# Kernel tuning notes

Measured on AMD Instinct MI355X. Metric: run time of the kernel, lower is better.

Reference implementation:

```python
import jax, jax.numpy as jnp
import numpy as np

B, S, H, NH, L, NS = 8, 4096, 768, 12, 2, 64
DH = H // NH
EPS = 1e-12


def _layer_norm(x, g, b):
    mu = jnp.mean(x, axis=-1, keepdims=True)
    var = jnp.mean((x - mu) ** 2, axis=-1, keepdims=True)
    return (x - mu) / jnp.sqrt(var + EPS) * g + b


def setup_inputs() -> dict:
    key = jax.random.key(0)
    ks = jax.random.split(key, 8)
    # sentence index per token: 64 equal contiguous sentences; position 0 is [CLS] in sentence 0
    sent_ind = jnp.broadcast_to((jnp.arange(S, dtype=jnp.int32) * NS) // S, (B, S)).astype(jnp.int32)
    start_layer = jax.random.normal(ks[0], (B, S, H), dtype=jnp.float32)
    init = lambda k, shape: (jax.random.normal(k, shape, dtype=jnp.float32) * 0.02)
    return {
        "sent_ind": sent_ind,
        "start_layer": start_layer,
        "Wq": init(ks[1], (L, H, H)), "bq": jnp.zeros((L, H), jnp.float32),
        "Wk": init(ks[2], (L, H, H)), "bk": jnp.zeros((L, H), jnp.float32),
        "Wv": init(ks[3], (L, H, H)), "bv": jnp.zeros((L, H), jnp.float32),
        "Wo": init(ks[4], (L, H, H)), "bo": jnp.zeros((L, H), jnp.float32),
        "ln_g": jnp.ones((L, H), jnp.float32), "ln_b": jnp.zeros((L, H), jnp.float32),
    }


def reference(sent_ind, start_layer, Wq, bq, Wk, bk, Wv, bv, Wo, bo, ln_g, ln_b):
    # ---- segment-mean pooling by sentence index (vectorized replacement of the python loops) ----
    onehot = (sent_ind[..., None] == jnp.arange(NS, dtype=sent_ind.dtype)).astype(start_layer.dtype)  # [B,S,NS]
    # the first [CLS] token is excluded from sentence 0's mean
    onehot = onehot.at[:, 0, :].set(0.0)
    sums = jnp.einsum('bsn,bsd->bnd', onehot, start_layer)          # [B,NS,H]
    counts = jnp.sum(onehot, axis=1)                                 # [B,NS]
    x = sums / counts[..., None]                                     # graph_vectors [B,NS,H]

    # ---- GAT layers: BertSelfAttention + GATSelfOutput(dense->gelu->LayerNorm), dropout=eval ----
    scale = 1.0 / (DH ** 0.5)
    for i in range(L):
        q = (x @ Wq[i] + bq[i]).reshape(B, NS, NH, DH)
        k = (x @ Wk[i] + bk[i]).reshape(B, NS, NH, DH)
        v = (x @ Wv[i] + bv[i]).reshape(B, NS, NH, DH)
        scores = jnp.einsum('bqhd,bkhd->bhqk', q, k) * scale
        probs = jax.nn.softmax(scores, axis=-1)
        ctx = jnp.einsum('bhqk,bkhd->bqhd', probs, v).reshape(B, NS, H)
        h = jax.nn.gelu(ctx @ Wo[i] + bo[i], approximate=False)
        x = _layer_norm(h, ln_g[i], ln_b[i])
    return x
```

## Files before the change

### kernel.cpp

```cpp
#include <hip/hip_runtime.h>
#include <hip/hip_bf16.h>

constexpr int cB  = 8;
constexpr int cS  = 4096;
constexpr int cH  = 768;
constexpr int cNH = 12;
constexpr int cL  = 2;
constexpr int cNS = 64;
constexpr int cDH = 64;
constexpr int cM  = cB * cNS;

typedef __attribute__((ext_vector_type(8))) short bf16x8;
typedef __attribute__((ext_vector_type(4))) float f32x4;

union PrepShared {
    struct { int cnt; int list[cS]; float ps[192][4]; } p;
    float T[2][64][65];
};

__global__ __launch_bounds__(512) void prep_kernel(
    const int* __restrict__ sent_ind, const float* __restrict__ sl,
    __hip_bfloat16* __restrict__ xb,
    const float* __restrict__ Wq, const float* __restrict__ Wk,
    const float* __restrict__ Wv, const float* __restrict__ Wo,
    __hip_bfloat16* __restrict__ wt)
{
    __shared__ PrepShared sh;
    int tid = threadIdx.x;

    if (blockIdx.x < (unsigned)cM) {
        int bn = blockIdx.x;
        int b = bn >> 6, n = bn & (cNS - 1);
        if (tid == 0) sh.p.cnt = 0;
        __syncthreads();
        const int* si = sent_ind + (size_t)b * cS;
        for (int s = tid; s < cS; s += 512)
            if (s != 0 && si[s] == n) { int p = atomicAdd(&sh.p.cnt, 1); sh.p.list[p] = s; }
        __syncthreads();
        int c = sh.p.cnt;
        int grp = tid >> 8;
        int t   = tid & 255;
        int c0 = c >> 1;
        int lo = grp ? c0 : 0;
        int hi = grp ? c  : c0;
        float s0 = 0.f, s1 = 0.f, s2 = 0.f, s3 = 0.f;
        if (t < 192) {
            const float* bbase = sl + (size_t)b * cS * cH;
            int col = t * 4;
            float4 a0 = {0.f, 0.f, 0.f, 0.f};
            float4 a1 = {0.f, 0.f, 0.f, 0.f};
            float4 a2 = {0.f, 0.f, 0.f, 0.f};
            float4 a3 = {0.f, 0.f, 0.f, 0.f};
            int i = lo;
            for (; i + 4 <= hi; i += 4) {
                float4 r0 = *(const float4*)(bbase + (size_t)sh.p.list[i + 0] * cH + col);
                float4 r1 = *(const float4*)(bbase + (size_t)sh.p.list[i + 1] * cH + col);
                float4 r2 = *(const float4*)(bbase + (size_t)sh.p.list[i + 2] * cH + col);
                float4 r3 = *(const float4*)(bbase + (size_t)sh.p.list[i + 3] * cH + col);
                a0.x += r0.x; a0.y += r0.y; a0.z += r0.z; a0.w += r0.w;
                a1.x += r1.x; a1.y += r1.y; a1.z += r1.z; a1.w += r1.w;
                a2.x += r2.x; a2.y += r2.y; a2.z += r2.z; a2.w += r2.w;
                a3.x += r3.x; a3.y += r3.y; a3.z += r3.z; a3.w += r3.w;
            }
            for (; i < hi; ++i) {
                float4 r0 = *(const float4*)(bbase + (size_t)sh.p.list[i] * cH + col);
                a0.x += r0.x; a0.y += r0.y; a0.z += r0.z; a0.w += r0.w;
            }
            s0 = a0.x + a1.x + a2.x + a3.x;
            s1 = a0.y + a1.y + a2.y + a3.y;
            s2 = a0.z + a1.z + a2.z + a3.z;
            s3 = a0.w + a1.w + a2.w + a3.w;
        }
        if (grp == 1 && t < 192) {
            sh.p.ps[t][0] = s0; sh.p.ps[t][1] = s1;
            sh.p.ps[t][2] = s2; sh.p.ps[t][3] = s3;
        }
        __syncthreads();
        if (grp == 0 && t < 192) {
            float inv = 1.0f / (float)c;
            __hip_bfloat16* xr = xb + (size_t)bn * cH + t * 4;
            xr[0] = __float2bfloat16((s0 + sh.p.ps[t][0]) * inv);
            xr[1] = __float2bfloat16((s1 + sh.p.ps[t][1]) * inv);
            xr[2] = __float2bfloat16((s2 + sh.p.ps[t][2]) * inv);
            xr[3] = __float2bfloat16((s3 + sh.p.ps[t][3]) * inv);
        }
    } else {
        int sub = tid >> 8;
        int t   = tid & 255;
        int bi = (blockIdx.x - cM) * 2 + sub;
        int bx = bi % 12, by = (bi / 12) % 12, mat = bi / 144;
        int layer = mat >> 2, which = mat & 3;
        const float* W = (which == 0 ? Wq : which == 1 ? Wk : which == 2 ? Wv : Wo)
                         + (size_t)layer * cH * cH;
        int k0 = by * 64, n0 = bx * 64;
        int r = t >> 2, cb = (t & 3) * 16;
        #pragma unroll
        for (int u = 0; u < 4; ++u) {
            float4 w4 = *(const float4*)(W + (size_t)(k0 + r) * cH + n0 + cb + u * 4);
            sh.T[sub][r][cb + u * 4 + 0] = w4.x; sh.T[sub][r][cb + u * 4 + 1] = w4.y;
            sh.T[sub][r][cb + u * 4 + 2] = w4.z; sh.T[sub][r][cb + u * 4 + 3] = w4.w;
        }
        __syncthreads();
        int nn = t >> 2, kseg = (t & 3) * 16;
        __hip_bfloat16 tmp[16] __attribute__((aligned(16)));
        #pragma unroll
        for (int j = 0; j < 16; ++j)
            tmp[j] = __float2bfloat16(sh.T[sub][kseg + j][nn]);
        __hip_bfloat16* dst = wt + ((size_t)mat * cH + n0 + nn) * cH + k0 + kseg;
        *(bf16x8*)(dst)     = *(const bf16x8*)(tmp);
        *(bf16x8*)(dst + 8) = *(const bf16x8*)(tmp + 8);
    }
}

struct AttnShared {
    float QP[cNS][cDH + 4];
    float Ks[cNS][cDH + 4];
    float Vt[cDH][cNS + 4];
};

__global__ __launch_bounds__(256) void qkvattn_kernel(
    const __hip_bfloat16* __restrict__ x_bf,
    const __hip_bfloat16* __restrict__ wqkv,
    const float* __restrict__ bq, const float* __restrict__ bk,
    const float* __restrict__ bv,
    __hip_bfloat16* __restrict__ ctx_bf)
{
    __shared__ AttnShared sh;
    int tid = threadIdx.x;
    int lane = tid & 63, wave = tid >> 6;
    int l15 = lane & 15, q4 = lane >> 4;
    int b = blockIdx.x / cNH, hh = blockIdx.x % cNH;

    const __hip_bfloat16* Arow[4];
    #pragma unroll
    for (int m = 0; m < 4; ++m)
        Arow[m] = x_bf + (size_t)(b * 64 + m * 16 + l15) * cH + q4 * 8;
    const __hip_bfloat16* Brow[3];
    int cmat[3], cnt_[3];
    #pragma unroll
    for (int j = 0; j < 3; ++j) {
        int c = wave * 3 + j;
        cmat[j] = c >> 2; cnt_[j] = c & 3;
        Brow[j] = wqkv + (size_t)cmat[j] * cH * cH
                       + (size_t)(hh * 64 + cnt_[j] * 16 + l15) * cH + q4 * 8;
    }

    f32x4 acc[3][4];
    #pragma unroll
    for (int j = 0; j < 3; ++j)
        #pragma unroll
        for (int m = 0; m < 4; ++m) acc[j][m] = (f32x4){0.f, 0.f, 0.f, 0.f};

    #pragma unroll 4
    for (int k0 = 0; k0 < cH; k0 += 32) {
        bf16x8 a[4], bb8[3];
        #pragma unroll
        for (int m = 0; m < 4; ++m) a[m] = *(const bf16x8*)(Arow[m] + k0);
        #pragma unroll
        for (int j = 0; j < 3; ++j) bb8[j] = *(const bf16x8*)(Brow[j] + k0);
        #pragma unroll
        for (int j = 0; j < 3; ++j)
            #pragma unroll
            for (int m = 0; m < 4; ++m)
                acc[j][m] = __builtin_amdgcn_mfma_f32_16x16x32_bf16(a[m], bb8[j], acc[j][m], 0, 0, 0);
    }

    const float scale = 0.125f;
    #pragma unroll
    for (int j = 0; j < 3; ++j) {
        int mat = cmat[j], nt = cnt_[j];
        int col_d = nt * 16 + l15;
        int col_g = hh * 64 + col_d;
        float bias = (mat == 0 ? bq : mat == 1 ? bk : bv)[col_g];
        #pragma unroll
        for (int m = 0; m < 4; ++m) {
            #pragma unroll
            for (int r = 0; r < 4; ++r) {
                int row_s = m * 16 + q4 * 4 + r;
                float v = acc[j][m][r] + bias;
                if (mat == 0)      sh.QP[row_s][col_d] = v * scale;
                else if (mat == 1) sh.Ks[row_s][col_d] = v;
                else               sh.Vt[col_d][row_s] = v;
            }
        }
    }
    __syncthreads();

    int tx = tid & 15, ty = tid >> 4;
    float accs[4][4] = {};
    for (int d = 0; d < cDH; d += 4) {
        float4 qv[4], kv[4];
        #pragma unroll
        for (int i = 0; i < 4; ++i) qv[i] = *(const float4*)&sh.QP[ty * 4 + i][d];
        #pragma unroll
        for (int j = 0; j < 4; ++j) kv[j] = *(const float4*)&sh.Ks[tx + j * 16][d];
        #pragma unroll
        for (int i = 0; i < 4; ++i)
            #pragma unroll
            for (int j = 0; j < 4; ++j)
                accs[i][j] += qv[i].x * kv[j].x + qv[i].y * kv[j].y +
                              qv[i].z * kv[j].z + qv[i].w * kv[j].w;
    }
    __syncthreads();
    #pragma unroll
    for (int i = 0; i < 4; ++i)
        #pragma unroll
        for (int j = 0; j < 4; ++j)
            sh.QP[ty * 4 + i][tx + j * 16] = accs[i][j];
    __syncthreads();

    {
        int row = tid >> 2, jq = tid & 3;
        float e[16];
        float m = -1e30f;
        #pragma unroll
        for (int c = 0; c < 16; ++c) { e[c] = sh.QP[row][jq * 16 + c]; m = fmaxf(m, e[c]); }
        m = fmaxf(m, __shfl_xor(m, 1));
        m = fmaxf(m, __shfl_xor(m, 2));
        float s = 0.f;
        #pragma unroll
        for (int c = 0; c < 16; ++c) { e[c] = __expf(e[c] - m); s += e[c]; }
        s += __shfl_xor(s, 1);
        s += __shfl_xor(s, 2);
        float inv = 1.0f / s;
        #pragma unroll
        for (int c = 0; c < 16; ++c) sh.QP[row][jq * 16 + c] = e[c] * inv;
    }
    __syncthreads();

    float acco[4][4] = {};
    for (int c = 0; c < cNS; c += 4) {
        float4 p4[4], vt4[4];
        #pragma unroll
        for (int i = 0; i < 4; ++i) p4[i] = *(const float4*)&sh.QP[ty * 4 + i][c];
        #pragma unroll
        for (int j = 0; j < 4; ++j) vt4[j] = *(const float4*)&sh.Vt[tx + j * 16][c];
        #pragma unroll
        for (int i = 0; i < 4; ++i)
            #pragma unroll
            for (int j = 0; j < 4; ++j)
                acco[i][j] += p4[i].x * vt4[j].x + p4[i].y * vt4[j].y +
                              p4[i].z * vt4[j].z + p4[i].w * vt4[j].w;
    }
    size_t base = ((size_t)b * cNS) * cH + hh * cDH;
    #pragma unroll
    for (int i = 0; i < 4; ++i)
        #pragma unroll
        for (int j = 0; j < 4; ++j)
            ctx_bf[base + (size_t)(ty * 4 + i) * cH + tx + j * 16] =
                __float2bfloat16(acco[i][j]);
}

__global__ __launch_bounds__(256) void ogemm_kernel(
    const __hip_bfloat16* __restrict__ A,
    const __hip_bfloat16* __restrict__ Wt,
    const float* __restrict__ bias,
    __hip_bfloat16* __restrict__ C)
{
    int lane = threadIdx.x & 63;
    int wave = threadIdx.x >> 6;
    int l15 = lane & 15, q4 = lane >> 4;
    int m0 = blockIdx.y * 64 + wave * 16;
    int n0 = blockIdx.x * 32;

    const __hip_bfloat16* Arow = A  + (size_t)(m0 + l15) * cH + q4 * 8;
    const __hip_bfloat16* Wr0  = Wt + (size_t)(n0 + l15) * cH + q4 * 8;
    const __hip_bfloat16* Wr1  = Wr0 + (size_t)16 * cH;

    f32x4 acc0 = {0.f, 0.f, 0.f, 0.f};
    f32x4 acc1 = {0.f, 0.f, 0.f, 0.f};
    #pragma unroll 8
    for (int k0 = 0; k0 < cH; k0 += 32) {
        bf16x8 a  = *(const bf16x8*)(Arow + k0);
        bf16x8 b0 = *(const bf16x8*)(Wr0 + k0);
        bf16x8 b1 = *(const bf16x8*)(Wr1 + k0);
        acc0 = __builtin_amdgcn_mfma_f32_16x16x32_bf16(a, b0, acc0, 0, 0, 0);
        acc1 = __builtin_amdgcn_mfma_f32_16x16x32_bf16(a, b1, acc1, 0, 0, 0);
    }
    #pragma unroll
    for (int nt = 0; nt < 2; ++nt) {
        const f32x4 acc = nt == 0 ? acc0 : acc1;
        int col = n0 + nt * 16 + l15;
        float bv = bias[col];
        #pragma unroll
        for (int r = 0; r < 4; ++r) {
            float v = acc[r] + bv;
            v = 0.5f * v * (1.0f + erff(v * 0.70710678118654752f));
            C[(size_t)(m0 + q4 * 4 + r) * cH + col] = __float2bfloat16(v);
        }
    }
}

__global__ __launch_bounds__(256) void ln_kernel(
    const __hip_bfloat16* __restrict__ h, const float* __restrict__ g,
    const float* __restrict__ bb, __hip_bfloat16* __restrict__ xb,
    float* __restrict__ outf)
{
    int row = blockIdx.x;
    const __hip_bfloat16* r = h + (size_t)row * cH;
    int tid = threadIdx.x;
    float v0 = __bfloat162float(r[tid]);
    float v1 = __bfloat162float(r[tid + 256]);
    float v2 = __bfloat162float(r[tid + 512]);
    float s = v0 + v1 + v2;
    __shared__ float red[4];
    #pragma unroll
    for (int o = 32; o; o >>= 1) s += __shfl_xor(s, o);
    if ((tid & 63) == 0) red[tid >> 6] = s;
    __syncthreads();
    float mu = (red[0] + red[1] + red[2] + red[3]) * (1.0f / 768.0f);
    float d0 = v0 - mu, d1 = v1 - mu, d2 = v2 - mu;
    float ss = d0 * d0 + d1 * d1 + d2 * d2;
    __syncthreads();
    #pragma unroll
    for (int o = 32; o; o >>= 1) ss += __shfl_xor(ss, o);
    if ((tid & 63) == 0) red[tid >> 6] = ss;
    __syncthreads();
    float var = (red[0] + red[1] + red[2] + red[3]) * (1.0f / 768.0f);
    float inv = rsqrtf(var + 1e-12f);
    float o0 = d0 * inv * g[tid]       + bb[tid];
    float o1 = d1 * inv * g[tid + 256] + bb[tid + 256];
    float o2 = d2 * inv * g[tid + 512] + bb[tid + 512];
    __hip_bfloat16* xr = xb + (size_t)row * cH;
    xr[tid]       = __float2bfloat16(o0);
    xr[tid + 256] = __float2bfloat16(o1);
    xr[tid + 512] = __float2bfloat16(o2);
    if (outf) {
        float* orow = outf + (size_t)row * cH;
        orow[tid] = o0; orow[tid + 256] = o1; orow[tid + 512] = o2;
    }
}

extern "C" void kernel_launch(void* const* d_in, const int* in_sizes, int n_in,
                              void* d_out, int out_size, void* d_ws, size_t ws_size,
                              hipStream_t stream) {
    const int*   sent_ind = (const int*)d_in[0];
    const float* start    = (const float*)d_in[1];
    const float* Wq = (const float*)d_in[2];
    const float* bq = (const float*)d_in[3];
    const float* Wk = (const float*)d_in[4];
    const float* bk = (const float*)d_in[5];
    const float* Wv = (const float*)d_in[6];
    const float* bv = (const float*)d_in[7];
    const float* Wo = (const float*)d_in[8];
    const float* bo = (const float*)d_in[9];
    const float* ln_g = (const float*)d_in[10];
    const float* ln_b = (const float*)d_in[11];
    float* out = (float*)d_out;

    char* w = (char*)d_ws;
    __hip_bfloat16* wt     = (__hip_bfloat16*)w;
    __hip_bfloat16* x_bf   = (__hip_bfloat16*)(w + 9437184);
    __hip_bfloat16* ctx_bf = (__hip_bfloat16*)(w + 9437184 + 786432);
    __hip_bfloat16* hb     = (__hip_bfloat16*)(w + 9437184 + 2 * 786432);

    prep_kernel<<<cM + 576, 512, 0, stream>>>(sent_ind, start, x_bf,
                                              Wq, Wk, Wv, Wo, wt);

    for (int i = 0; i < cL; ++i) {
        const __hip_bfloat16* wqkv = wt + (size_t)(i * 4) * cH * cH;
        const __hip_bfloat16* wto  = wt + (size_t)(i * 4 + 3) * cH * cH;
        qkvattn_kernel<<<cB * cNH, 256, 0, stream>>>(
            x_bf, wqkv, bq + (size_t)i * cH, bk + (size_t)i * cH, bv + (size_t)i * cH,
            ctx_bf);
        ogemm_kernel<<<dim3(24, 8), 256, 0, stream>>>(
            ctx_bf, wto, bo + (size_t)i * cH, hb);
        ln_kernel<<<cM, 256, 0, stream>>>(
            hb, ln_g + (size_t)i * cH, ln_b + (size_t)i * cH,
            x_bf, (i == cL - 1) ? out : nullptr);
    }
}
```

Measured before the change: 285.1 us.

## Fuse all stages into one cooperative persistent kernel with grid syncs

Replaces the seven separate launches (prep, then qkv-attention, output GEMM and layernorm per layer) with a single cooperative kernel of 512 blocks of 256 threads, using grid.sync between stages. The pooling and weight-transpose work are now done with 256 threads per block instead of 512. The aim is to remove per-launch overhead and inter-kernel gaps. The cost is that grid-wide barriers idle most blocks during the small attention and GEMM stages, and the pooling loses thread parallelism. The old multi-launch path is kept as a fallback if the cooperative launch fails.

```diff
diff --git a/kernel.cpp b/kernel.cpp
--- a/kernel.cpp
+++ b/kernel.cpp
@@ -1,5 +1,8 @@
 #include <hip/hip_runtime.h>
 #include <hip/hip_bf16.h>
+#include <hip/hip_cooperative_groups.h>
+
+namespace cg = cooperative_groups;
 
 constexpr int cB  = 8;
 constexpr int cS  = 4096;
@@ -12,6 +15,335 @@
 
 typedef __attribute__((ext_vector_type(8))) short bf16x8;
 typedef __attribute__((ext_vector_type(4))) float f32x4;
+
+struct AttnShared {
+    float QP[cNS][cDH + 4];
+    float Ks[cNS][cDH + 4];
+    float Vt[cDH][cNS + 4];
+};
+
+__device__ __forceinline__ void qkvattn_body(
+    const __hip_bfloat16* __restrict__ x_bf,
+    const __hip_bfloat16* __restrict__ wqkv,
+    const float* __restrict__ bq, const float* __restrict__ bk,
+    const float* __restrict__ bv,
+    __hip_bfloat16* __restrict__ ctx_bf,
+    int b, int hh, AttnShared& sh)
+{
+    int tid = threadIdx.x;
+    int lane = tid & 63, wave = tid >> 6;
+    int l15 = lane & 15, q4 = lane >> 4;
+
+    const __hip_bfloat16* Arow[4];
+    #pragma unroll
+    for (int m = 0; m < 4; ++m)
+        Arow[m] = x_bf + (size_t)(b * 64 + m * 16 + l15) * cH + q4 * 8;
+    const __hip_bfloat16* Brow[3];
+    int cmat[3], cnt_[3];
+    #pragma unroll
+    for (int j = 0; j < 3; ++j) {
+        int c = wave * 3 + j;
+        cmat[j] = c >> 2; cnt_[j] = c & 3;
+        Brow[j] = wqkv + (size_t)cmat[j] * cH * cH
+                       + (size_t)(hh * 64 + cnt_[j] * 16 + l15) * cH + q4 * 8;
+    }
+
+    f32x4 acc[3][4];
+    #pragma unroll
+    for (int j = 0; j < 3; ++j)
+        #pragma unroll
+        for (int m = 0; m < 4; ++m) acc[j][m] = (f32x4){0.f, 0.f, 0.f, 0.f};
+
+    #pragma unroll 4
+    for (int k0 = 0; k0 < cH; k0 += 32) {
+        bf16x8 a[4], bb8[3];
+        #pragma unroll
+        for (int m = 0; m < 4; ++m) a[m] = *(const bf16x8*)(Arow[m] + k0);
+        #pragma unroll
+        for (int j = 0; j < 3; ++j) bb8[j] = *(const bf16x8*)(Brow[j] + k0);
+        #pragma unroll
+        for (int j = 0; j < 3; ++j)
+            #pragma unroll
+            for (int m = 0; m < 4; ++m)
+                acc[j][m] = __builtin_amdgcn_mfma_f32_16x16x32_bf16(a[m], bb8[j], acc[j][m], 0, 0, 0);
+    }
+
+    const float scale = 0.125f;
+    #pragma unroll
+    for (int j = 0; j < 3; ++j) {
+        int mat = cmat[j], nt = cnt_[j];
+        int col_d = nt * 16 + l15;
+        int col_g = hh * 64 + col_d;
+        float bias = (mat == 0 ? bq : mat == 1 ? bk : bv)[col_g];
+        #pragma unroll
+        for (int m = 0; m < 4; ++m) {
+            #pragma unroll
+            for (int r = 0; r < 4; ++r) {
+                int row_s = m * 16 + q4 * 4 + r;
+                float v = acc[j][m][r] + bias;
+                if (mat == 0)      sh.QP[row_s][col_d] = v * scale;
+                else if (mat == 1) sh.Ks[row_s][col_d] = v;
+                else               sh.Vt[col_d][row_s] = v;
+            }
+        }
+    }
+    __syncthreads();
+
+    int tx = tid & 15, ty = tid >> 4;
+    float accs[4][4] = {};
+    for (int d = 0; d < cDH; d += 4) {
+        float4 qv[4], kv[4];
+        #pragma unroll
+        for (int i = 0; i < 4; ++i) qv[i] = *(const float4*)&sh.QP[ty * 4 + i][d];
+        #pragma unroll
+        for (int j = 0; j < 4; ++j) kv[j] = *(const float4*)&sh.Ks[tx + j * 16][d];
+        #pragma unroll
+        for (int i = 0; i < 4; ++i)
+            #pragma unroll
+            for (int j = 0; j < 4; ++j)
+                accs[i][j] += qv[i].x * kv[j].x + qv[i].y * kv[j].y +
+                              qv[i].z * kv[j].z + qv[i].w * kv[j].w;
+    }
+    __syncthreads();
+    #pragma unroll
+    for (int i = 0; i < 4; ++i)
+        #pragma unroll
+        for (int j = 0; j < 4; ++j)
+            sh.QP[ty * 4 + i][tx + j * 16] = accs[i][j];
+    __syncthreads();
+
+    {
+        int row = tid >> 2, jq = tid & 3;
+        float e[16];
+        float m = -1e30f;
+        #pragma unroll
+        for (int c = 0; c < 16; ++c) { e[c] = sh.QP[row][jq * 16 + c]; m = fmaxf(m, e[c]); }
+        m = fmaxf(m, __shfl_xor(m, 1));
+        m = fmaxf(m, __shfl_xor(m, 2));
+        float s = 0.f;
+        #pragma unroll
+        for (int c = 0; c < 16; ++c) { e[c] = __expf(e[c] - m); s += e[c]; }
+        s += __shfl_xor(s, 1);
+        s += __shfl_xor(s, 2);
+        float inv = 1.0f / s;
+        #pragma unroll
+        for (int c = 0; c < 16; ++c) sh.QP[row][jq * 16 + c] = e[c] * inv;
+    }
+    __syncthreads();
+
+    float acco[4][4] = {};
+    for (int c = 0; c < cNS; c += 4) {
+        float4 p4[4], vt4[4];
+        #pragma unroll
+        for (int i = 0; i < 4; ++i) p4[i] = *(const float4*)&sh.QP[ty * 4 + i][c];
+        #pragma unroll
+        for (int j = 0; j < 4; ++j) vt4[j] = *(const float4*)&sh.Vt[tx + j * 16][c];
+        #pragma unroll
+        for (int i = 0; i < 4; ++i)
+            #pragma unroll
+            for (int j = 0; j < 4; ++j)
+                acco[i][j] += p4[i].x * vt4[j].x + p4[i].y * vt4[j].y +
+                              p4[i].z * vt4[j].z + p4[i].w * vt4[j].w;
+    }
+    size_t base = ((size_t)b * cNS) * cH + hh * cDH;
+    #pragma unroll
+    for (int i = 0; i < 4; ++i)
+        #pragma unroll
+        for (int j = 0; j < 4; ++j)
+            ctx_bf[base + (size_t)(ty * 4 + i) * cH + tx + j * 16] =
+                __float2bfloat16(acco[i][j]);
+}
+
+__device__ __forceinline__ void ogemm_body(
+    const __hip_bfloat16* __restrict__ A,
+    const __hip_bfloat16* __restrict__ Wt,
+    const float* __restrict__ bias,
+    __hip_bfloat16* __restrict__ C,
+    int gx, int gy)
+{
+    int lane = threadIdx.x & 63;
+    int wave = threadIdx.x >> 6;
+    int l15 = lane & 15, q4 = lane >> 4;
+    int m0 = gy * 64 + wave * 16;
+    int n0 = gx * 32;
+
+    const __hip_bfloat16* Arow = A  + (size_t)(m0 + l15) * cH + q4 * 8;
+    const __hip_bfloat16* Wr0  = Wt + (size_t)(n0 + l15) * cH + q4 * 8;
+    const __hip_bfloat16* Wr1  = Wr0 + (size_t)16 * cH;
+
+    f32x4 acc0 = {0.f, 0.f, 0.f, 0.f};
+    f32x4 acc1 = {0.f, 0.f, 0.f, 0.f};
+    #pragma unroll 8
+    for (int k0 = 0; k0 < cH; k0 += 32) {
+        bf16x8 a  = *(const bf16x8*)(Arow + k0);
+        bf16x8 b0 = *(const bf16x8*)(Wr0 + k0);
+        bf16x8 b1 = *(const bf16x8*)(Wr1 + k0);
+        acc0 = __builtin_amdgcn_mfma_f32_16x16x32_bf16(a, b0, acc0, 0, 0, 0);
+        acc1 = __builtin_amdgcn_mfma_f32_16x16x32_bf16(a, b1, acc1, 0, 0, 0);
+    }
+    #pragma unroll
+    for (int nt = 0; nt < 2; ++nt) {
+        const f32x4 acc = nt == 0 ? acc0 : acc1;
+        int col = n0 + nt * 16 + l15;
+        float bv = bias[col];
+        #pragma unroll
+        for (int r = 0; r < 4; ++r) {
+            float v = acc[r] + bv;
+            v = 0.5f * v * (1.0f + erff(v * 0.70710678118654752f));
+            C[(size_t)(m0 + q4 * 4 + r) * cH + col] = __float2bfloat16(v);
+        }
+    }
+}
+
+__device__ __forceinline__ void ln_body(
+    const __hip_bfloat16* __restrict__ h, const float* __restrict__ g,
+    const float* __restrict__ bb, __hip_bfloat16* __restrict__ xb,
+    float* __restrict__ outf, int row)
+{
+    const __hip_bfloat16* r = h + (size_t)row * cH;
+    int tid = threadIdx.x;
+    float v0 = __bfloat162float(r[tid]);
+    float v1 = __bfloat162float(r[tid + 256]);
+    float v2 = __bfloat162float(r[tid + 512]);
+    float s = v0 + v1 + v2;
+    __shared__ float red[4];
+    #pragma unroll
+    for (int o = 32; o; o >>= 1) s += __shfl_xor(s, o);
+    if ((tid & 63) == 0) red[tid >> 6] = s;
+    __syncthreads();
+    float mu = (red[0] + red[1] + red[2] + red[3]) * (1.0f / 768.0f);
+    float d0 = v0 - mu, d1 = v1 - mu, d2 = v2 - mu;
+    float ss = d0 * d0 + d1 * d1 + d2 * d2;
+    __syncthreads();
+    #pragma unroll
+    for (int o = 32; o; o >>= 1) ss += __shfl_xor(ss, o);
+    if ((tid & 63) == 0) red[tid >> 6] = ss;
+    __syncthreads();
+    float var = (red[0] + red[1] + red[2] + red[3]) * (1.0f / 768.0f);
+    float inv = rsqrtf(var + 1e-12f);
+    float o0 = d0 * inv * g[tid]       + bb[tid];
+    float o1 = d1 * inv * g[tid + 256] + bb[tid + 256];
+    float o2 = d2 * inv * g[tid + 512] + bb[tid + 512];
+    __hip_bfloat16* xr = xb + (size_t)row * cH;
+    xr[tid]       = __float2bfloat16(o0);
+    xr[tid + 256] = __float2bfloat16(o1);
+    xr[tid + 512] = __float2bfloat16(o2);
+    if (outf) {
+        float* orow = outf + (size_t)row * cH;
+        orow[tid] = o0; orow[tid + 256] = o1; orow[tid + 512] = o2;
+    }
+}
+
+union MegaShared {
+    struct { int cnt; int list[cS]; } p;
+    float T[64][65];
+    AttnShared a;
+};
+
+__global__ __launch_bounds__(256, 2) void mega_kernel(
+    const int* __restrict__ sent_ind, const float* __restrict__ sl,
+    const float* __restrict__ Wq, const float* __restrict__ Wk,
+    const float* __restrict__ Wv, const float* __restrict__ Wo,
+    const float* __restrict__ bq, const float* __restrict__ bk,
+    const float* __restrict__ bv, const float* __restrict__ bo,
+    const float* __restrict__ ln_g, const float* __restrict__ ln_b,
+    __hip_bfloat16* __restrict__ wt, __hip_bfloat16* __restrict__ x_bf,
+    __hip_bfloat16* __restrict__ ctx_bf, __hip_bfloat16* __restrict__ hb,
+    float* __restrict__ out)
+{
+    cg::grid_group grid = cg::this_grid();
+    __shared__ MegaShared sh;
+    const int tid = threadIdx.x;
+    const int bid = blockIdx.x;
+
+    {
+        int b = bid >> 6, n = bid & (cNS - 1);
+        if (tid == 0) sh.p.cnt = 0;
+        __syncthreads();
+        const int* si = sent_ind + (size_t)b * cS;
+        for (int s = tid; s < cS; s += 256)
+            if (s != 0 && si[s] == n) { int p = atomicAdd(&sh.p.cnt, 1); sh.p.list[p] = s; }
+        __syncthreads();
+        int c = sh.p.cnt;
+        if (tid < 192) {
+            const float* bbase = sl + (size_t)b * cS * cH;
+            int col = tid * 4;
+            float4 a0 = {0.f, 0.f, 0.f, 0.f};
+            float4 a1 = {0.f, 0.f, 0.f, 0.f};
+            float4 a2 = {0.f, 0.f, 0.f, 0.f};
+            float4 a3 = {0.f, 0.f, 0.f, 0.f};
+            int i = 0;
+            for (; i + 4 <= c; i += 4) {
+                float4 r0 = *(const float4*)(bbase + (size_t)sh.p.list[i + 0] * cH + col);
+                float4 r1 = *(const float4*)(bbase + (size_t)sh.p.list[i + 1] * cH + col);
+                float4 r2 = *(const float4*)(bbase + (size_t)sh.p.list[i + 2] * cH + col);
+                float4 r3 = *(const float4*)(bbase + (size_t)sh.p.list[i + 3] * cH + col);
+                a0.x += r0.x; a0.y += r0.y; a0.z += r0.z; a0.w += r0.w;
+                a1.x += r1.x; a1.y += r1.y; a1.z += r1.z; a1.w += r1.w;
+                a2.x += r2.x; a2.y += r2.y; a2.z += r2.z; a2.w += r2.w;
+                a3.x += r3.x; a3.y += r3.y; a3.z += r3.z; a3.w += r3.w;
+            }
+            for (; i < c; ++i) {
+                float4 r0 = *(const float4*)(bbase + (size_t)sh.p.list[i] * cH + col);
+                a0.x += r0.x; a0.y += r0.y; a0.z += r0.z; a0.w += r0.w;
+            }
+            float inv = 1.0f / (float)c;
+            __hip_bfloat16* xr = x_bf + (size_t)bid * cH + col;
+            xr[0] = __float2bfloat16((a0.x + a1.x + a2.x + a3.x) * inv);
+            xr[1] = __float2bfloat16((a0.y + a1.y + a2.y + a3.y) * inv);
+            xr[2] = __float2bfloat16((a0.z + a1.z + a2.z + a3.z) * inv);
+            xr[3] = __float2bfloat16((a0.w + a1.w + a2.w + a3.w) * inv);
+        }
+        __syncthreads();
+    }
+
+    for (int bi = bid; bi < 1152; bi += cM) {
+        int bx = bi % 12, by = (bi / 12) % 12, mat = bi / 144;
+        int layer = mat >> 2, which = mat & 3;
+        const float* W = (which == 0 ? Wq : which == 1 ? Wk : which == 2 ? Wv : Wo)
+                         + (size_t)layer * cH * cH;
+        int k0 = by * 64, n0 = bx * 64;
+        int r = tid >> 2, cb = (tid & 3) * 16;
+        #pragma unroll
+        for (int u = 0; u < 4; ++u) {
+            float4 w4 = *(const float4*)(W + (size_t)(k0 + r) * cH + n0 + cb + u * 4);
+            sh.T[r][cb + u * 4 + 0] = w4.x; sh.T[r][cb + u * 4 + 1] = w4.y;
+            sh.T[r][cb + u * 4 + 2] = w4.z; sh.T[r][cb + u * 4 + 3] = w4.w;
+        }
+        __syncthreads();
+        int nn = tid >> 2, kseg = (tid & 3) * 16;
+        __hip_bfloat16 tmp[16] __attribute__((aligned(16)));
+        #pragma unroll
+        for (int j = 0; j < 16; ++j)
+            tmp[j] = __float2bfloat16(sh.T[kseg + j][nn]);
+        __hip_bfloat16* dst = wt + ((size_t)mat * cH + n0 + nn) * cH + k0 + kseg;
+        *(bf16x8*)(dst)     = *(const bf16x8*)(tmp);
+        *(bf16x8*)(dst + 8) = *(const bf16x8*)(tmp + 8);
+        __syncthreads();
+    }
+    grid.sync();
+
+    for (int layer = 0; layer < cL; ++layer) {
+        const __hip_bfloat16* wqkv = wt + (size_t)(layer * 4) * cH * cH;
+        const __hip_bfloat16* wto  = wt + (size_t)(layer * 4 + 3) * cH * cH;
+
+        if (bid < cB * cNH)
+            qkvattn_body(x_bf, wqkv,
+                         bq + (size_t)layer * cH, bk + (size_t)layer * cH,
+                         bv + (size_t)layer * cH, ctx_bf,
+                         bid / cNH, bid % cNH, sh.a);
+        grid.sync();
+
+        if (bid < 192)
+            ogemm_body(ctx_bf, wto, bo + (size_t)layer * cH, hb,
+                       bid % 24, bid / 24);
+        grid.sync();
+
+        ln_body(hb, ln_g + (size_t)layer * cH, ln_b + (size_t)layer * cH,
+                x_bf, (layer == cL - 1) ? out : nullptr, bid);
+        if (layer != cL - 1) grid.sync();
+    }
+}
 
 union PrepShared {
     struct { int cnt; int list[cS]; float ps[192][4]; } p;
@@ -112,12 +444,6 @@
     }
 }
 
-struct AttnShared {
-    float QP[cNS][cDH + 4];
-    float Ks[cNS][cDH + 4];
-    float Vt[cDH][cNS + 4];
-};
-
 __global__ __launch_bounds__(256) void qkvattn_kernel(
     const __hip_bfloat16* __restrict__ x_bf,
     const __hip_bfloat16* __restrict__ wqkv,
@@ -126,129 +452,8 @@
     __hip_bfloat16* __restrict__ ctx_bf)
 {
     __shared__ AttnShared sh;
-    int tid = threadIdx.x;
-    int lane = tid & 63, wave = tid >> 6;
-    int l15 = lane & 15, q4 = lane >> 4;
-    int b = blockIdx.x / cNH, hh = blockIdx.x % cNH;
-
-    const __hip_bfloat16* Arow[4];
-    #pragma unroll
-    for (int m = 0; m < 4; ++m)
-        Arow[m] = x_bf + (size_t)(b * 64 + m * 16 + l15) * cH + q4 * 8;
-    const __hip_bfloat16* Brow[3];
-    int cmat[3], cnt_[3];
-    #pragma unroll
-    for (int j = 0; j < 3; ++j) {
-        int c = wave * 3 + j;
-        cmat[j] = c >> 2; cnt_[j] = c & 3;
-        Brow[j] = wqkv + (size_t)cmat[j] * cH * cH
-                       + (size_t)(hh * 64 + cnt_[j] * 16 + l15) * cH + q4 * 8;
-    }
-
-    f32x4 acc[3][4];
-    #pragma unroll
-    for (int j = 0; j < 3; ++j)
-        #pragma unroll
-        for (int m = 0; m < 4; ++m) acc[j][m] = (f32x4){0.f, 0.f, 0.f, 0.f};
-
-    #pragma unroll 4
-    for (int k0 = 0; k0 < cH; k0 += 32) {
-        bf16x8 a[4], bb8[3];
-        #pragma unroll
-        for (int m = 0; m < 4; ++m) a[m] = *(const bf16x8*)(Arow[m] + k0);
-        #pragma unroll
-        for (int j = 0; j < 3; ++j) bb8[j] = *(const bf16x8*)(Brow[j] + k0);
-        #pragma unroll
-        for (int j = 0; j < 3; ++j)
-            #pragma unroll
-            for (int m = 0; m < 4; ++m)
-                acc[j][m] = __builtin_amdgcn_mfma_f32_16x16x32_bf16(a[m], bb8[j], acc[j][m], 0, 0, 0);
-    }
-
-    const float scale = 0.125f;
-    #pragma unroll
-    for (int j = 0; j < 3; ++j) {
-        int mat = cmat[j], nt = cnt_[j];
-        int col_d = nt * 16 + l15;
-        int col_g = hh * 64 + col_d;
-        float bias = (mat == 0 ? bq : mat == 1 ? bk : bv)[col_g];
-        #pragma unroll
-        for (int m = 0; m < 4; ++m) {
-            #pragma unroll
-            for (int r = 0; r < 4; ++r) {
-                int row_s = m * 16 + q4 * 4 + r;
-                float v = acc[j][m][r] + bias;
-                if (mat == 0)      sh.QP[row_s][col_d] = v * scale;
-                else if (mat == 1) sh.Ks[row_s][col_d] = v;
-                else               sh.Vt[col_d][row_s] = v;
-            }
-        }
-    }
-    __syncthreads();
-
-    int tx = tid & 15, ty = tid >> 4;
-    float accs[4][4] = {};
-    for (int d = 0; d < cDH; d += 4) {
-        float4 qv[4], kv[4];
-        #pragma unroll
-        for (int i = 0; i < 4; ++i) qv[i] = *(const float4*)&sh.QP[ty * 4 + i][d];
-        #pragma unroll
-        for (int j = 0; j < 4; ++j) kv[j] = *(const float4*)&sh.Ks[tx + j * 16][d];
-        #pragma unroll
-        for (int i = 0; i < 4; ++i)
-            #pragma unroll
-            for (int j = 0; j < 4; ++j)
-                accs[i][j] += qv[i].x * kv[j].x + qv[i].y * kv[j].y +
-                              qv[i].z * kv[j].z + qv[i].w * kv[j].w;
-    }
-    __syncthreads();
-    #pragma unroll
-    for (int i = 0; i < 4; ++i)
-        #pragma unroll
-        for (int j = 0; j < 4; ++j)
-            sh.QP[ty * 4 + i][tx + j * 16] = accs[i][j];
-    __syncthreads();
-
-    {
-        int row = tid >> 2, jq = tid & 3;
-        float e[16];
-        float m = -1e30f;
-        #pragma unroll
-        for (int c = 0; c < 16; ++c) { e[c] = sh.QP[row][jq * 16 + c]; m = fmaxf(m, e[c]); }
-        m = fmaxf(m, __shfl_xor(m, 1));
-        m = fmaxf(m, __shfl_xor(m, 2));
-        float s = 0.f;
-        #pragma unroll
-        for (int c = 0; c < 16; ++c) { e[c] = __expf(e[c] - m); s += e[c]; }
-        s += __shfl_xor(s, 1);
-        s += __shfl_xor(s, 2);
-        float inv = 1.0f / s;
-        #pragma unroll
-        for (int c = 0; c < 16; ++c) sh.QP[row][jq * 16 + c] = e[c] * inv;
-    }
-    __syncthreads();
-
-    float acco[4][4] = {};
-    for (int c = 0; c < cNS; c += 4) {
-        float4 p4[4], vt4[4];
-        #pragma unroll
-        for (int i = 0; i < 4; ++i) p4[i] = *(const float4*)&sh.QP[ty * 4 + i][c];
-        #pragma unroll
-        for (int j = 0; j < 4; ++j) vt4[j] = *(const float4*)&sh.Vt[tx + j * 16][c];
-        #pragma unroll
-        for (int i = 0; i < 4; ++i)
-            #pragma unroll
-            for (int j = 0; j < 4; ++j)
-                acco[i][j] += p4[i].x * vt4[j].x + p4[i].y * vt4[j].y +
-                              p4[i].z * vt4[j].z + p4[i].w * vt4[j].w;
-    }
-    size_t base = ((size_t)b * cNS) * cH + hh * cDH;
-    #pragma unroll
-    for (int i = 0; i < 4; ++i)
-        #pragma unroll
-        for (int j = 0; j < 4; ++j)
-            ctx_bf[base + (size_t)(ty * 4 + i) * cH + tx + j * 16] =
-                __float2bfloat16(acco[i][j]);
+    qkvattn_body(x_bf, wqkv, bq, bk, bv, ctx_bf,
+                 blockIdx.x / cNH, blockIdx.x % cNH, sh);
 }
 
 __global__ __launch_bounds__(256) void ogemm_kernel(
@@ -257,38 +462,7 @@
     const float* __restrict__ bias,
     __hip_bfloat16* __restrict__ C)
 {
-    int lane = threadIdx.x & 63;
-    int wave = threadIdx.x >> 6;
-    int l15 = lane & 15, q4 = lane >> 4;
-    int m0 = blockIdx.y * 64 + wave * 16;
-    int n0 = blockIdx.x * 32;
-
-    const __hip_bfloat16* Arow = A  + (size_t)(m0 + l15) * cH + q4 * 8;
-    const __hip_bfloat16* Wr0  = Wt + (size_t)(n0 + l15) * cH + q4 * 8;
-    const __hip_bfloat16* Wr1  = Wr0 + (size_t)16 * cH;
-
-    f32x4 acc0 = {0.f, 0.f, 0.f, 0.f};
-    f32x4 acc1 = {0.f, 0.f, 0.f, 0.f};
-    #pragma unroll 8
-    for (int k0 = 0; k0 < cH; k0 += 32) {
-        bf16x8 a  = *(const bf16x8*)(Arow + k0);
-        bf16x8 b0 = *(const bf16x8*)(Wr0 + k0);
-        bf16x8 b1 = *(const bf16x8*)(Wr1 + k0);
-        acc0 = __builtin_amdgcn_mfma_f32_16x16x32_bf16(a, b0, acc0, 0, 0, 0);
-        acc1 = __builtin_amdgcn_mfma_f32_16x16x32_bf16(a, b1, acc1, 0, 0, 0);
-    }
-    #pragma unroll
-    for (int nt = 0; nt < 2; ++nt) {
-        const f32x4 acc = nt == 0 ? acc0 : acc1;
-        int col = n0 + nt * 16 + l15;
-        float bv = bias[col];
-        #pragma unroll
-        for (int r = 0; r < 4; ++r) {
-            float v = acc[r] + bv;
-            v = 0.5f * v * (1.0f + erff(v * 0.70710678118654752f));
-            C[(size_t)(m0 + q4 * 4 + r) * cH + col] = __float2bfloat16(v);
-        }
-    }
+    ogemm_body(A, Wt, bias, C, blockIdx.x, blockIdx.y);
 }
 
 __global__ __launch_bounds__(256) void ln_kernel(
@@ -296,39 +470,7 @@
     const float* __restrict__ bb, __hip_bfloat16* __restrict__ xb,
     float* __restrict__ outf)
 {
-    int row = blockIdx.x;
-    const __hip_bfloat16* r = h + (size_t)row * cH;
-    int tid = threadIdx.x;
-    float v0 = __bfloat162float(r[tid]);
-    float v1 = __bfloat162float(r[tid + 256]);
-    float v2 = __bfloat162float(r[tid + 512]);
-    float s = v0 + v1 + v2;
-    __shared__ float red[4];
-    #pragma unroll
-    for (int o = 32; o; o >>= 1) s += __shfl_xor(s, o);
-    if ((tid & 63) == 0) red[tid >> 6] = s;
-    __syncthreads();
-    float mu = (red[0] + red[1] + red[2] + red[3]) * (1.0f / 768.0f);
-    float d0 = v0 - mu, d1 = v1 - mu, d2 = v2 - mu;
-    float ss = d0 * d0 + d1 * d1 + d2 * d2;
-    __syncthreads();
-    #pragma unroll
-    for (int o = 32; o; o >>= 1) ss += __shfl_xor(ss, o);
-    if ((tid & 63) == 0) red[tid >> 6] = ss;
-    __syncthreads();
-    float var = (red[0] + red[1] + red[2] + red[3]) * (1.0f / 768.0f);
-    float inv = rsqrtf(var + 1e-12f);
-    float o0 = d0 * inv * g[tid]       + bb[tid];
-    float o1 = d1 * inv * g[tid + 256] + bb[tid + 256];
-    float o2 = d2 * inv * g[tid + 512] + bb[tid + 512];
-    __hip_bfloat16* xr = xb + (size_t)row * cH;
-    xr[tid]       = __float2bfloat16(o0);
-    xr[tid + 256] = __float2bfloat16(o1);
-    xr[tid + 512] = __float2bfloat16(o2);
-    if (outf) {
-        float* orow = outf + (size_t)row * cH;
-        orow[tid] = o0; orow[tid + 256] = o1; orow[tid + 512] = o2;
-    }
+    ln_body(h, g, bb, xb, outf, blockIdx.x);
 }
 
 extern "C" void kernel_launch(void* const* d_in, const int* in_sizes, int n_in,
@@ -354,19 +496,30 @@
     __hip_bfloat16* ctx_bf = (__hip_bfloat16*)(w + 9437184 + 786432);
     __hip_bfloat16* hb     = (__hip_bfloat16*)(w + 9437184 + 2 * 786432);
 
-    prep_kernel<<<cM + 576, 512, 0, stream>>>(sent_ind, start, x_bf,
-                                              Wq, Wk, Wv, Wo, wt);
-
-    for (int i = 0; i < cL; ++i) {
-        const __hip_bfloat16* wqkv = wt + (size_t)(i * 4) * cH * cH;
-        const __hip_bfloat16* wto  = wt + (size_t)(i * 4 + 3) * cH * cH;
-        qkvattn_kernel<<<cB * cNH, 256, 0, stream>>>(
-            x_bf, wqkv, bq + (size_t)i * cH, bk + (size_t)i * cH, bv + (size_t)i * cH,
-            ctx_bf);
-        ogemm_kernel<<<dim3(24, 8), 256, 0, stream>>>(
-            ctx_bf, wto, bo + (size_t)i * cH, hb);
-        ln_kernel<<<cM, 256, 0, stream>>>(
-            hb, ln_g + (size_t)i * cH, ln_b + (size_t)i * cH,
-            x_bf, (i == cL - 1) ? out : nullptr);
-    }
-}
+    void* kargs[] = {
+        (void*)&sent_ind, (void*)&start,
+        (void*)&Wq, (void*)&Wk, (void*)&Wv, (void*)&Wo,
+        (void*)&bq, (void*)&bk, (void*)&bv, (void*)&bo,
+        (void*)&ln_g, (void*)&ln_b,
+        (void*)&wt, (void*)&x_bf, (void*)&ctx_bf, (void*)&hb, (void*)&out
+    };
+    hipError_t err = hipLaunchCooperativeKernel(
+        (const void*)mega_kernel, dim3(cM), dim3(256), kargs, 0, stream);
+
+    if (err != hipSuccess) {
+        prep_kernel<<<cM + 576, 512, 0, stream>>>(sent_ind, start, x_bf,
+                                                  Wq, Wk, Wv, Wo, wt);
+        for (int i = 0; i < cL; ++i) {
+            const __hip_bfloat16* wqkv = wt + (size_t)(i * 4) * cH * cH;
+            const __hip_bfloat16* wto  = wt + (size_t)(i * 4 + 3) * cH * cH;
+            qkvattn_kernel<<<cB * cNH, 256, 0, stream>>>(
+                x_bf, wqkv, bq + (size_t)i * cH, bk + (size_t)i * cH,
+                bv + (size_t)i * cH, ctx_bf);
+            ogemm_kernel<<<dim3(24, 8), 256, 0, stream>>>(
+                ctx_bf, wto, bo + (size_t)i * cH, hb);
+            ln_kernel<<<cM, 256, 0, stream>>>(
+                hb, ln_g + (size_t)i * cH, ln_b + (size_t)i * cH,
+                x_bf, (i == cL - 1) ? out : nullptr);
+        }
+    }
+}
```

After: 632.2 us. 2.22x slower.

## Fuse output GEMM with LayerNorm via last-block atomic counter per row tile

Applied to the files above, without the earlier changes.

Adds a fused kernel that computes the output projection with GELU and then, using a per-row-tile atomic counter, lets the last finishing block of each 64-row tile run LayerNorm on that tile. This removes one kernel launch per layer and the launch gap between the GEMM and LayerNorm. In exchange, only 8 blocks do the LayerNorm work, serialized at the tail of each tile. The fused path runs only if the workspace is large enough to hold the counters, which prep_kernel zeroes.

```diff
diff --git a/kernel.cpp b/kernel.cpp
--- a/kernel.cpp
+++ b/kernel.cpp
@@ -12,6 +12,15 @@
 
 typedef __attribute__((ext_vector_type(8))) short bf16x8;
 typedef __attribute__((ext_vector_type(4))) float f32x4;
+typedef __attribute__((ext_vector_type(4))) unsigned short u16x4;
+
+__device__ __forceinline__ float b2f(unsigned short u) {
+    union { float f; unsigned int i; } x; x.i = (unsigned int)u << 16; return x.f;
+}
+__device__ __forceinline__ unsigned short f2b(float f) {
+    __hip_bfloat16 h = __float2bfloat16(f);
+    return *(unsigned short*)&h;
+}
 
 union PrepShared {
     struct { int cnt; int list[cS]; float ps[192][4]; } p;
@@ -23,10 +32,13 @@
     __hip_bfloat16* __restrict__ xb,
     const float* __restrict__ Wq, const float* __restrict__ Wk,
     const float* __restrict__ Wv, const float* __restrict__ Wo,
-    __hip_bfloat16* __restrict__ wt)
+    __hip_bfloat16* __restrict__ wt,
+    int* __restrict__ lncnt)
 {
     __shared__ PrepShared sh;
     int tid = threadIdx.x;
+
+    if (lncnt && blockIdx.x == 0 && tid < 16) lncnt[tid] = 0;
 
     if (blockIdx.x < (unsigned)cM) {
         int bn = blockIdx.x;
@@ -251,6 +263,123 @@
                 __float2bfloat16(acco[i][j]);
 }
 
+__global__ __launch_bounds__(256) void ogemm_ln_kernel(
+    const __hip_bfloat16* __restrict__ A,
+    const __hip_bfloat16* __restrict__ Wt,
+    const float* __restrict__ bias,
+    __hip_bfloat16* __restrict__ C,
+    const float* __restrict__ g, const float* __restrict__ bb,
+    __hip_bfloat16* __restrict__ xb,
+    float* __restrict__ outf,
+    int* __restrict__ cnt)
+{
+    int tid  = threadIdx.x;
+    int lane = tid & 63;
+    int wave = tid >> 6;
+    int l15 = lane & 15, q4 = lane >> 4;
+    int gx = blockIdx.x, gy = blockIdx.y;
+    int m0 = gy * 64 + wave * 16;
+    int n0 = gx * 32;
+
+    const __hip_bfloat16* Arow = A  + (size_t)(m0 + l15) * cH + q4 * 8;
+    const __hip_bfloat16* Wr0  = Wt + (size_t)(n0 + l15) * cH + q4 * 8;
+    const __hip_bfloat16* Wr1  = Wr0 + (size_t)16 * cH;
+
+    f32x4 acc0 = {0.f, 0.f, 0.f, 0.f};
+    f32x4 acc1 = {0.f, 0.f, 0.f, 0.f};
+    #pragma unroll 8
+    for (int k0 = 0; k0 < cH; k0 += 32) {
+        bf16x8 a  = *(const bf16x8*)(Arow + k0);
+        bf16x8 b0 = *(const bf16x8*)(Wr0 + k0);
+        bf16x8 b1 = *(const bf16x8*)(Wr1 + k0);
+        acc0 = __builtin_amdgcn_mfma_f32_16x16x32_bf16(a, b0, acc0, 0, 0, 0);
+        acc1 = __builtin_amdgcn_mfma_f32_16x16x32_bf16(a, b1, acc1, 0, 0, 0);
+    }
+    #pragma unroll
+    for (int nt = 0; nt < 2; ++nt) {
+        const f32x4 acc = nt == 0 ? acc0 : acc1;
+        int col = n0 + nt * 16 + l15;
+        float bv = bias[col];
+        #pragma unroll
+        for (int r = 0; r < 4; ++r) {
+            float v = acc[r] + bv;
+            v = 0.5f * v * (1.0f + erff(v * 0.70710678118654752f));
+            C[(size_t)(m0 + q4 * 4 + r) * cH + col] = __float2bfloat16(v);
+        }
+    }
+
+    __shared__ int isfin;
+    __syncthreads();
+    if (tid == 0) {
+        __threadfence();
+        isfin = (atomicAdd(&cnt[gy], 1) == 23);
+    }
+    __syncthreads();
+    if (!isfin) return;
+    __threadfence();
+
+    float gv[12], bv2[12];
+    {
+        const float* gp = g  + lane * 12;
+        const float* bp = bb + lane * 12;
+        #pragma unroll
+        for (int j = 0; j < 3; ++j) {
+            float4 g4 = *(const float4*)(gp + j * 4);
+            float4 b4 = *(const float4*)(bp + j * 4);
+            gv[j * 4 + 0] = g4.x; gv[j * 4 + 1] = g4.y;
+            gv[j * 4 + 2] = g4.z; gv[j * 4 + 3] = g4.w;
+            bv2[j * 4 + 0] = b4.x; bv2[j * 4 + 1] = b4.y;
+            bv2[j * 4 + 2] = b4.z; bv2[j * 4 + 3] = b4.w;
+        }
+    }
+    for (int r = wave; r < 64; r += 4) {
+        int row = gy * 64 + r;
+        const unsigned short* hr =
+            (const unsigned short*)(C + (size_t)row * cH) + lane * 12;
+        float v[12];
+        #pragma unroll
+        for (int j = 0; j < 3; ++j) {
+            u16x4 q = *(const u16x4*)(hr + j * 4);
+            v[j * 4 + 0] = b2f(q[0]); v[j * 4 + 1] = b2f(q[1]);
+            v[j * 4 + 2] = b2f(q[2]); v[j * 4 + 3] = b2f(q[3]);
+        }
+        float s = 0.f;
+        #pragma unroll
+        for (int j = 0; j < 12; ++j) s += v[j];
+        #pragma unroll
+        for (int o = 32; o; o >>= 1) s += __shfl_xor(s, o);
+        float mu = s * (1.0f / 768.0f);
+        float ss = 0.f;
+        #pragma unroll
+        for (int j = 0; j < 12; ++j) { v[j] -= mu; ss += v[j] * v[j]; }
+        #pragma unroll
+        for (int o = 32; o; o >>= 1) ss += __shfl_xor(ss, o);
+        float var = ss * (1.0f / 768.0f);
+        float inv = rsqrtf(var + 1e-12f);
+        float o12[12];
+        #pragma unroll
+        for (int j = 0; j < 12; ++j) o12[j] = v[j] * inv * gv[j] + bv2[j];
+
+        unsigned short* xr = (unsigned short*)(xb + (size_t)row * cH) + lane * 12;
+        #pragma unroll
+        for (int j = 0; j < 3; ++j) {
+            u16x4 q;
+            q[0] = f2b(o12[j * 4 + 0]); q[1] = f2b(o12[j * 4 + 1]);
+            q[2] = f2b(o12[j * 4 + 2]); q[3] = f2b(o12[j * 4 + 3]);
+            *(u16x4*)(xr + j * 4) = q;
+        }
+        if (outf) {
+            float* orow = outf + (size_t)row * cH + lane * 12;
+            #pragma unroll
+            for (int j = 0; j < 3; ++j) {
+                float4 o4 = { o12[j * 4 + 0], o12[j * 4 + 1],
+                              o12[j * 4 + 2], o12[j * 4 + 3] };
+                *(float4*)(orow + j * 4) = o4;
+            }
+        }
+    }
+}
+
 __global__ __launch_bounds__(256) void ogemm_kernel(
     const __hip_bfloat16* __restrict__ A,
     const __hip_bfloat16* __restrict__ Wt,
@@ -353,9 +482,13 @@
     __hip_bfloat16* x_bf   = (__hip_bfloat16*)(w + 9437184);
     __hip_bfloat16* ctx_bf = (__hip_bfloat16*)(w + 9437184 + 786432);
     __hip_bfloat16* hb     = (__hip_bfloat16*)(w + 9437184 + 2 * 786432);
+    const size_t base_sz   = 9437184 + 3 * (size_t)786432;
+
+    bool fused = ws_size >= base_sz + 256;
+    int* lncnt = fused ? (int*)(w + base_sz) : nullptr;
 
     prep_kernel<<<cM + 576, 512, 0, stream>>>(sent_ind, start, x_bf,
-                                              Wq, Wk, Wv, Wo, wt);
+                                              Wq, Wk, Wv, Wo, wt, lncnt);
 
     for (int i = 0; i < cL; ++i) {
         const __hip_bfloat16* wqkv = wt + (size_t)(i * 4) * cH * cH;
@@ -363,10 +496,17 @@
         qkvattn_kernel<<<cB * cNH, 256, 0, stream>>>(
             x_bf, wqkv, bq + (size_t)i * cH, bk + (size_t)i * cH, bv + (size_t)i * cH,
             ctx_bf);
-        ogemm_kernel<<<dim3(24, 8), 256, 0, stream>>>(
-            ctx_bf, wto, bo + (size_t)i * cH, hb);
-        ln_kernel<<<cM, 256, 0, stream>>>(
-            hb, ln_g + (size_t)i * cH, ln_b + (size_t)i * cH,
-            x_bf, (i == cL - 1) ? out : nullptr);
-    }
-}
+        if (fused) {
+            ogemm_ln_kernel<<<dim3(24, 8), 256, 0, stream>>>(
+                ctx_bf, wto, bo + (size_t)i * cH, hb,
+                ln_g + (size_t)i * cH, ln_b + (size_t)i * cH,
+                x_bf, (i == cL - 1) ? out : nullptr, lncnt + i * 8);
+        } else {
+            ogemm_kernel<<<dim3(24, 8), 256, 0, stream>>>(
+                ctx_bf, wto, bo + (size_t)i * cH, hb);
+            ln_kernel<<<cM, 256, 0, stream>>>(
+                hb, ln_g + (size_t)i * cH, ln_b + (size_t)i * cH,
+                x_bf, (i == cL - 1) ? out : nullptr);
+        }
+    }
+}
```

Measured after the change: 324.5 us. 13.9% more time.

## Fuse output projection GEMM with GELU and LayerNorm into one kernel

Applied to the files above, without the earlier changes.

Merges the output-projection GEMM+GELU kernel and the LayerNorm kernel into a single kernel. Each 512-thread block computes 32 full rows of the output in LDS, then normalizes them in place. This removes one launch and the global round trip of the intermediate h buffer. The cost is that the grid shrinks from 192 blocks to 16, which greatly reduces parallelism on a GPU with many CUs, and each wave now holds 12 accumulators and 12 weight fragments in registers.

```diff
diff --git a/kernel.cpp b/kernel.cpp
--- a/kernel.cpp
+++ b/kernel.cpp
@@ -12,6 +12,15 @@
 
 typedef __attribute__((ext_vector_type(8))) short bf16x8;
 typedef __attribute__((ext_vector_type(4))) float f32x4;
+typedef __attribute__((ext_vector_type(4))) unsigned short u16x4;
+
+__device__ __forceinline__ float b2f(unsigned short u) {
+    union { float f; unsigned int i; } x; x.i = (unsigned int)u << 16; return x.f;
+}
+__device__ __forceinline__ unsigned short f2b(float f) {
+    __hip_bfloat16 h = __float2bfloat16(f);
+    return *(unsigned short*)&h;
+}
 
 union PrepShared {
     struct { int cnt; int list[cS]; float ps[192][4]; } p;
@@ -251,83 +260,116 @@
                 __float2bfloat16(acco[i][j]);
 }
 
-__global__ __launch_bounds__(256) void ogemm_kernel(
+__global__ __launch_bounds__(512) void ogemm_ln_kernel(
     const __hip_bfloat16* __restrict__ A,
     const __hip_bfloat16* __restrict__ Wt,
     const float* __restrict__ bias,
-    __hip_bfloat16* __restrict__ C)
-{
-    int lane = threadIdx.x & 63;
-    int wave = threadIdx.x >> 6;
-    int l15 = lane & 15, q4 = lane >> 4;
-    int m0 = blockIdx.y * 64 + wave * 16;
-    int n0 = blockIdx.x * 32;
-
-    const __hip_bfloat16* Arow = A  + (size_t)(m0 + l15) * cH + q4 * 8;
-    const __hip_bfloat16* Wr0  = Wt + (size_t)(n0 + l15) * cH + q4 * 8;
-    const __hip_bfloat16* Wr1  = Wr0 + (size_t)16 * cH;
-
-    f32x4 acc0 = {0.f, 0.f, 0.f, 0.f};
-    f32x4 acc1 = {0.f, 0.f, 0.f, 0.f};
-    #pragma unroll 8
-    for (int k0 = 0; k0 < cH; k0 += 32) {
-        bf16x8 a  = *(const bf16x8*)(Arow + k0);
-        bf16x8 b0 = *(const bf16x8*)(Wr0 + k0);
-        bf16x8 b1 = *(const bf16x8*)(Wr1 + k0);
-        acc0 = __builtin_amdgcn_mfma_f32_16x16x32_bf16(a, b0, acc0, 0, 0, 0);
-        acc1 = __builtin_amdgcn_mfma_f32_16x16x32_bf16(a, b1, acc1, 0, 0, 0);
-    }
-    #pragma unroll
-    for (int nt = 0; nt < 2; ++nt) {
-        const f32x4 acc = nt == 0 ? acc0 : acc1;
-        int col = n0 + nt * 16 + l15;
-        float bv = bias[col];
-        #pragma unroll
-        for (int r = 0; r < 4; ++r) {
-            float v = acc[r] + bv;
-            v = 0.5f * v * (1.0f + erff(v * 0.70710678118654752f));
-            C[(size_t)(m0 + q4 * 4 + r) * cH + col] = __float2bfloat16(v);
-        }
-    }
-}
-
-__global__ __launch_bounds__(256) void ln_kernel(
-    const __hip_bfloat16* __restrict__ h, const float* __restrict__ g,
-    const float* __restrict__ bb, __hip_bfloat16* __restrict__ xb,
+    const float* __restrict__ g, const float* __restrict__ bb,
+    __hip_bfloat16* __restrict__ xb,
     float* __restrict__ outf)
 {
-    int row = blockIdx.x;
-    const __hip_bfloat16* r = h + (size_t)row * cH;
-    int tid = threadIdx.x;
-    float v0 = __bfloat162float(r[tid]);
-    float v1 = __bfloat162float(r[tid + 256]);
-    float v2 = __bfloat162float(r[tid + 512]);
-    float s = v0 + v1 + v2;
-    __shared__ float red[4];
-    #pragma unroll
-    for (int o = 32; o; o >>= 1) s += __shfl_xor(s, o);
-    if ((tid & 63) == 0) red[tid >> 6] = s;
+    __shared__ unsigned short hs[32][776];
+    int tid  = threadIdx.x;
+    int lane = tid & 63;
+    int wave = tid >> 6;
+    int l15 = lane & 15, q4 = lane >> 4;
+    int msub = wave & 1;
+    int nb   = (wave >> 1) * 192;
+    int r0 = blockIdx.x * 32;
+    int m0 = r0 + msub * 16;
+
+    const __hip_bfloat16* Arow = A  + (size_t)(m0 + l15) * cH + q4 * 8;
+    const __hip_bfloat16* Wr   = Wt + (size_t)(nb + l15) * cH + q4 * 8;
+
+    f32x4 acc[12];
+    #pragma unroll
+    for (int j = 0; j < 12; ++j) acc[j] = (f32x4){0.f, 0.f, 0.f, 0.f};
+
+    #pragma unroll 2
+    for (int k0 = 0; k0 < cH; k0 += 32) {
+        bf16x8 a = *(const bf16x8*)(Arow + k0);
+        bf16x8 bw[12];
+        #pragma unroll
+        for (int j = 0; j < 12; ++j)
+            bw[j] = *(const bf16x8*)(Wr + (size_t)j * 16 * cH + k0);
+        #pragma unroll
+        for (int j = 0; j < 12; ++j)
+            acc[j] = __builtin_amdgcn_mfma_f32_16x16x32_bf16(a, bw[j], acc[j], 0, 0, 0);
+    }
+
+    #pragma unroll
+    for (int j = 0; j < 12; ++j) {
+        int col = nb + j * 16 + l15;
+        float bv = bias[col];
+        #pragma unroll
+        for (int r = 0; r < 4; ++r) {
+            float v = acc[j][r] + bv;
+            v = 0.5f * v * (1.0f + erff(v * 0.70710678118654752f));
+            hs[msub * 16 + q4 * 4 + r][col] = f2b(v);
+        }
+    }
     __syncthreads();
-    float mu = (red[0] + red[1] + red[2] + red[3]) * (1.0f / 768.0f);
-    float d0 = v0 - mu, d1 = v1 - mu, d2 = v2 - mu;
-    float ss = d0 * d0 + d1 * d1 + d2 * d2;
-    __syncthreads();
-    #pragma unroll
-    for (int o = 32; o; o >>= 1) ss += __shfl_xor(ss, o);
-    if ((tid & 63) == 0) red[tid >> 6] = ss;
-    __syncthreads();
-    float var = (red[0] + red[1] + red[2] + red[3]) * (1.0f / 768.0f);
-    float inv = rsqrtf(var + 1e-12f);
-    float o0 = d0 * inv * g[tid]       + bb[tid];
-    float o1 = d1 * inv * g[tid + 256] + bb[tid + 256];
-    float o2 = d2 * inv * g[tid + 512] + bb[tid + 512];
-    __hip_bfloat16* xr = xb + (size_t)row * cH;
-    xr[tid]       = __float2bfloat16(o0);
-    xr[tid + 256] = __float2bfloat16(o1);
-    xr[tid + 512] = __float2bfloat16(o2);
-    if (outf) {
-        float* orow = outf + (size_t)row * cH;
-        orow[tid] = o0; orow[tid + 256] = o1; orow[tid + 512] = o2;
+
+    float gv[12], bv2[12];
+    {
+        const float* gp = g  + lane * 12;
+        const float* bp = bb + lane * 12;
+        #pragma unroll
+        for (int j = 0; j < 3; ++j) {
+            float4 g4 = *(const float4*)(gp + j * 4);
+            float4 b4 = *(const float4*)(bp + j * 4);
+            gv[j * 4 + 0] = g4.x; gv[j * 4 + 1] = g4.y;
+            gv[j * 4 + 2] = g4.z; gv[j * 4 + 3] = g4.w;
+            bv2[j * 4 + 0] = b4.x; bv2[j * 4 + 1] = b4.y;
+            bv2[j * 4 + 2] = b4.z; bv2[j * 4 + 3] = b4.w;
+        }
+    }
+    #pragma unroll
+    for (int rr = 0; rr < 4; ++rr) {
+        int lrow = wave * 4 + rr;
+        int grow = r0 + lrow;
+        const unsigned short* hr = &hs[lrow][lane * 12];
+        float v[12];
+        #pragma unroll
+        for (int j = 0; j < 3; ++j) {
+            u16x4 q = *(const u16x4*)(hr + j * 4);
+            v[j * 4 + 0] = b2f(q[0]); v[j * 4 + 1] = b2f(q[1]);
+            v[j * 4 + 2] = b2f(q[2]); v[j * 4 + 3] = b2f(q[3]);
+        }
+        float s = 0.f;
+        #pragma unroll
+        for (int j = 0; j < 12; ++j) s += v[j];
+        #pragma unroll
+        for (int o = 32; o; o >>= 1) s += __shfl_xor(s, o);
+        float mu = s * (1.0f / 768.0f);
+        float ss = 0.f;
+        #pragma unroll
+        for (int j = 0; j < 12; ++j) { v[j] -= mu; ss += v[j] * v[j]; }
+        #pragma unroll
+        for (int o = 32; o; o >>= 1) ss += __shfl_xor(ss, o);
+        float var = ss * (1.0f / 768.0f);
+        float inv = rsqrtf(var + 1e-12f);
+        float o12[12];
+        #pragma unroll
+        for (int j = 0; j < 12; ++j) o12[j] = v[j] * inv * gv[j] + bv2[j];
+
+        unsigned short* xr = (unsigned short*)(xb + (size_t)grow * cH) + lane * 12;
+        #pragma unroll
+        for (int j = 0; j < 3; ++j) {
+            u16x4 q;
+            q[0] = f2b(o12[j * 4 + 0]); q[1] = f2b(o12[j * 4 + 1]);
+            q[2] = f2b(o12[j * 4 + 2]); q[3] = f2b(o12[j * 4 + 3]);
+            *(u16x4*)(xr + j * 4) = q;
+        }
+        if (outf) {
+            float* orow = outf + (size_t)grow * cH + lane * 12;
+            #pragma unroll
+            for (int j = 0; j < 3; ++j) {
+                float4 o4 = { o12[j * 4 + 0], o12[j * 4 + 1],
+                              o12[j * 4 + 2], o12[j * 4 + 3] };
+                *(float4*)(orow + j * 4) = o4;
+            }
+        }
     }
 }
 
@@ -352,7 +394,6 @@
     __hip_bfloat16* wt     = (__hip_bfloat16*)w;
     __hip_bfloat16* x_bf   = (__hip_bfloat16*)(w + 9437184);
     __hip_bfloat16* ctx_bf = (__hip_bfloat16*)(w + 9437184 + 786432);
-    __hip_bfloat16* hb     = (__hip_bfloat16*)(w + 9437184 + 2 * 786432);
 
     prep_kernel<<<cM + 576, 512, 0, stream>>>(sent_ind, start, x_bf,
                                               Wq, Wk, Wv, Wo, wt);
@@ -363,10 +404,9 @@
         qkvattn_kernel<<<cB * cNH, 256, 0, stream>>>(
             x_bf, wqkv, bq + (size_t)i * cH, bk + (size_t)i * cH, bv + (size_t)i * cH,
             ctx_bf);
-        ogemm_kernel<<<dim3(24, 8), 256, 0, stream>>>(
-            ctx_bf, wto, bo + (size_t)i * cH, hb);
-        ln_kernel<<<cM, 256, 0, stream>>>(
-            hb, ln_g + (size_t)i * cH, ln_b + (size_t)i * cH,
+        ogemm_ln_kernel<<<16, 512, 0, stream>>>(
+            ctx_bf, wto, bo + (size_t)i * cH,
+            ln_g + (size_t)i * cH, ln_b + (size_t)i * cH,
             x_bf, (i == cL - 1) ? out : nullptr);
     }
 }
```

Result: slower. 407.0 us (+42.8%).
